# Optimization experiments

Measured on AMD Instinct MI355X. Metric: run time of the kernel, lower is better.

Reference implementation:

```python
import jax, jax.numpy as jnp
import numpy as np

B, N, D, K, H = 32768, 17, 2, 3, 64


def _mlp_params(key, n, d_in, d_hid, d_out):
    k1, k2, k3, k4 = jax.random.split(key, 4)
    W1 = jax.random.normal(k1, (n, d_in, d_hid), jnp.float32) / np.sqrt(d_in)
    b1 = jnp.zeros((n, d_hid), jnp.float32)
    W2 = jax.random.normal(k2, (n, d_hid, d_out), jnp.float32) / np.sqrt(d_hid)
    b2 = jnp.zeros((n, d_out), jnp.float32)
    return W1, b1, W2, b2


def setup_inputs() -> dict:
    key = jax.random.key(0)
    kp, kk, kw, kb = jax.random.split(key, 4)
    pred_pts = jax.random.normal(kp, (B, N, D), jnp.float32)
    kW1, kb1, kW2, kb2 = _mlp_params(kk, N, D, H, K)            # k_nets
    wW1, wb1, wW2, wb2 = _mlp_params(kw, N, D, H, K)            # weight_nets
    bW1, bb1, bW2, bb2 = _mlp_params(kb, N, D, 2 * H, K * 2 * D)  # basis_nets
    return dict(pred_pts=pred_pts,
                kW1=kW1, kb1=kb1, kW2=kW2, kb2=kb2,
                wW1=wW1, wb1=wb1, wW2=wW2, wb2=wb2,
                bW1=bW1, bb1=bb1, bW2=bW2, bb2=bb2)


def _per_joint_mlp(x, W1, b1, W2, b2):
    # x: [B,N,D]; W1: [N,D,Hd]; W2: [N,Hd,O]
    h = jax.nn.relu(jnp.einsum('bnd,ndh->bnh', x, W1) + b1[None])
    return jnp.einsum('bnh,nho->bno', h, W2) + b2[None]


def reference(pred_pts, kW1, kb1, kW2, kb2, wW1, wb1, wW2, wb2, bW1, bb1, bW2, bb2):
    Bc, Nc, Dc = pred_pts.shape
    Kc = kW2.shape[-1]

    # k-selection head (eval mode: argmax, +1)
    k_logits = _per_joint_mlp(pred_pts, kW1, kb1, kW2, kb2)      # [B,N,K]
    k_js = jnp.argmax(k_logits, axis=-1) + 1                     # [B,N] int

    # mixture weights
    w = jax.nn.softmax(_per_joint_mlp(pred_pts, wW1, wb1, wW2, wb2), axis=-1)  # [B,N,K]

    # basis parameters: mu, sigma = exp(log_sigma)
    params = _per_joint_mlp(pred_pts, bW1, bb1, bW2, bb2).reshape(Bc, Nc, Kc, 2 * Dc)
    mu = params[..., :Dc]                                         # [B,N,K,D]
    sigma = jnp.exp(params[..., Dc:])                             # [B,N,K,D]

    # top-k selection by descending weight (indices are constants w.r.t. grad)
    idx = jnp.argsort(-w, axis=-1)                                # [B,N,K]
    mu_top = jnp.take_along_axis(mu, idx[..., None], axis=2)      # [B,N,K,D]
    sigma_top = jnp.take_along_axis(sigma, idx[..., None], axis=2)
    mask = jnp.arange(Kc)[None, None, :] < k_js[..., None]        # [B,N,K] bool

    # pack float outputs: weights + selected (mu, sigma) -> [B,N,K,1+2D]
    out = jnp.concatenate([w[..., None], mu_top, sigma_top], axis=-1)
    return out, k_js, mask
```

## Files before the change

### kernel.cpp

```cpp
#include <hip/hip_runtime.h>
#include <cmath>

#define NBATCH 32768
#define NJOINT 17
#define OUT0_ELEMS (NBATCH * NJOINT * 15)
#define KJS_OFF    OUT0_ELEMS
#define MASK_OFF   (KJS_OFF + NBATCH * NJOINT)

#define WN_STRIDE 774
#define WS_DOUBLES (NJOINT * WN_STRIDE)
#define TILE_B   128

__device__ __forceinline__ float sel3f(int i, float a, float b, float c) {
    return (i == 0) ? a : ((i == 1) ? b : c);
}

__global__ void cvt_weights_f64(
    const float* __restrict__ kW1, const float* __restrict__ kb1,
    const float* __restrict__ kW2, const float* __restrict__ kb2,
    const float* __restrict__ wW1, const float* __restrict__ wb1,
    const float* __restrict__ wW2, const float* __restrict__ wb2,
    double* __restrict__ dws)
{
    const int n = blockIdx.x;
    double* o = dws + (size_t)n * WN_STRIDE;
    for (int i = threadIdx.x; i < WN_STRIDE; i += blockDim.x) {
        int j = i;
        const float* W1 = kW1; const float* b1 = kb1;
        const float* W2 = kW2; const float* b2 = kb2;
        if (j >= 387) { j -= 387; W1 = wW1; b1 = wb1; W2 = wW2; b2 = wb2; }
        float v;
        if (j < 128)      v = W1[n * 128 + j];
        else if (j < 192) v = b1[n * 64 + (j - 128)];
        else if (j < 384) v = W2[n * 192 + (j - 192)];
        else              v = b2[n * 3 + (j - 384)];
        o[i] = (double)v;
    }
}

__device__ __forceinline__ void mlp64_ws_2(
    const double* __restrict__ gws,
    double xA0, double xA1, double xB0, double xB1,
    double& lA0, double& lA1, double& lA2,
    double& lB0, double& lB1, double& lB2)
{
    const double* W1a = gws;
    const double* W1b = gws + 64;
    const double* b1  = gws + 128;
    const double* W2  = gws + 192;
    lA0 = gws[384]; lA1 = gws[385]; lA2 = gws[386];
    lB0 = gws[384]; lB1 = gws[385]; lB2 = gws[386];
    #pragma unroll 4
    for (int h = 0; h < 64; ++h) {
        const double wa = W1a[h], wb = W1b[h], bb = b1[h];
        const double w0 = W2[h * 3 + 0], w1 = W2[h * 3 + 1], w2 = W2[h * 3 + 2];
        double hvA = fmax(fma(xA1, wb, fma(xA0, wa, bb)), 0.0);
        double hvB = fmax(fma(xB1, wb, fma(xB0, wa, bb)), 0.0);
        lA0 = fma(hvA, w0, lA0); lB0 = fma(hvB, w0, lB0);
        lA1 = fma(hvA, w1, lA1); lB1 = fma(hvB, w1, lB1);
        lA2 = fma(hvA, w2, lA2); lB2 = fma(hvB, w2, lB2);
    }
}

__device__ __forceinline__ void mlp64_cvt_2(
    const float* __restrict__ W1, const float* __restrict__ b1f,
    const float* __restrict__ W2f, const float* __restrict__ b2f, int n,
    double xA0, double xA1, double xB0, double xB1,
    double& lA0, double& lA1, double& lA2,
    double& lB0, double& lB1, double& lB2)
{
    const float* W1a = W1 + n * 128;
    const float* W1b = W1a + 64;
    const float* b1  = b1f + n * 64;
    const float* W2  = W2f + n * 192;
    lA0 = (double)b2f[n * 3 + 0]; lB0 = lA0;
    lA1 = (double)b2f[n * 3 + 1]; lB1 = lA1;
    lA2 = (double)b2f[n * 3 + 2]; lB2 = lA2;
    #pragma unroll 4
    for (int h = 0; h < 64; ++h) {
        const double wa = (double)W1a[h], wb = (double)W1b[h], bb = (double)b1[h];
        const double w0 = (double)W2[h * 3 + 0], w1 = (double)W2[h * 3 + 1],
                     w2 = (double)W2[h * 3 + 2];
        double hvA = fmax(fma(xA1, wb, fma(xA0, wa, bb)), 0.0);
        double hvB = fmax(fma(xB1, wb, fma(xB0, wa, bb)), 0.0);
        lA0 = fma(hvA, w0, lA0); lB0 = fma(hvB, w0, lB0);
        lA1 = fma(hvA, w1, lA1); lB1 = fma(hvB, w1, lB1);
        lA2 = fma(hvA, w2, lA2); lB2 = fma(hvB, w2, lB2);
    }
}

__device__ __forceinline__ void decide(
    double kl0, double kl1, double kl2,
    double wl0, double wl1, double wl2,
    int& kj, int& i0, int& i1, int& i2,
    float& p0, float& p1, float& p2)
{
    kj = 0;
    {
        double m = kl0;
        if (kl1 > m) { m = kl1; kj = 1; }
        if (kl2 > m) { kj = 2; }
    }
    i0 = 0;
    {
        double m = wl0;
        if (wl1 > m) { m = wl1; i0 = 1; }
        if (wl2 > m) { i0 = 2; }
    }
    const int ia = (i0 == 0) ? 1 : 0;
    const int ib = (i0 == 2) ? 1 : 2;
    const double wa = ia ? wl1 : wl0;
    const double wb = (ib == 1) ? wl1 : wl2;
    i1 = (wb > wa) ? ib : ia;
    i2 = (wb > wa) ? ia : ib;

    const double mw = fmax(fmax(wl0, wl1), wl2);
    const float e0 = __expf((float)(wl0 - mw));
    const float e1 = __expf((float)(wl1 - mw));
    const float e2 = __expf((float)(wl2 - mw));
    const float inv = 1.0f / (e0 + e1 + e2);
    p0 = e0 * inv; p1 = e1 * inv; p2 = e2 * inv;
}

__device__ __forceinline__ void epilogue(
    const float acc[12], int i0, int i1, int i2,
    float p0, float p1, float p2, float r[15])
{
    r[0]  = p0; r[5] = p1; r[10] = p2;
    r[1]  = sel3f(i0, acc[0], acc[4], acc[8]);
    r[2]  = sel3f(i0, acc[1], acc[5], acc[9]);
    r[3]  = __expf(sel3f(i0, acc[2], acc[6], acc[10]));
    r[4]  = __expf(sel3f(i0, acc[3], acc[7], acc[11]));
    r[6]  = sel3f(i1, acc[0], acc[4], acc[8]);
    r[7]  = sel3f(i1, acc[1], acc[5], acc[9]);
    r[8]  = __expf(sel3f(i1, acc[2], acc[6], acc[10]));
    r[9]  = __expf(sel3f(i1, acc[3], acc[7], acc[11]));
    r[11] = sel3f(i2, acc[0], acc[4], acc[8]);
    r[12] = sel3f(i2, acc[1], acc[5], acc[9]);
    r[13] = __expf(sel3f(i2, acc[2], acc[6], acc[10]));
    r[14] = __expf(sel3f(i2, acc[3], acc[7], acc[11]));
}

template<bool USE_WS>
__device__ __forceinline__ void compute2(
    int n, float xA0f, float xA1f, float xB0f, float xB1f,
    const float* __restrict__ kW1, const float* __restrict__ kb1,
    const float* __restrict__ kW2, const float* __restrict__ kb2,
    const float* __restrict__ wW1, const float* __restrict__ wb1,
    const float* __restrict__ wW2, const float* __restrict__ wb2,
    const float* __restrict__ bW1, const float* __restrict__ bb1,
    const float* __restrict__ bW2, const float* __restrict__ bb2,
    const double* __restrict__ dws,
    float rA[15], float rB[15], int& kjA, int& kjB)
{
    const double xA0 = (double)xA0f, xA1 = (double)xA1f;
    const double xB0 = (double)xB0f, xB1 = (double)xB1f;

    double klA0, klA1, klA2, klB0, klB1, klB2;
    double wlA0, wlA1, wlA2, wlB0, wlB1, wlB2;
    if constexpr (USE_WS) {
        const double* Wn = dws + (size_t)n * WN_STRIDE;
        mlp64_ws_2(Wn,       xA0, xA1, xB0, xB1, klA0, klA1, klA2, klB0, klB1, klB2);
        mlp64_ws_2(Wn + 387, xA0, xA1, xB0, xB1, wlA0, wlA1, wlA2, wlB0, wlB1, wlB2);
    } else {
        mlp64_cvt_2(kW1, kb1, kW2, kb2, n, xA0, xA1, xB0, xB1,
                    klA0, klA1, klA2, klB0, klB1, klB2);
        mlp64_cvt_2(wW1, wb1, wW2, wb2, n, xA0, xA1, xB0, xB1,
                    wlA0, wlA1, wlA2, wlB0, wlB1, wlB2);
    }

    int i0A, i1A, i2A, i0B, i1B, i2B;
    float p0A, p1A, p2A, p0B, p1B, p2B;
    decide(klA0, klA1, klA2, wlA0, wlA1, wlA2, kjA, i0A, i1A, i2A, p0A, p1A, p2A);
    decide(klB0, klB1, klB2, wlB0, wlB1, wlB2, kjB, i0B, i1B, i2B, p0B, p1B, p2B);

    float accA[12], accB[12];
    {
        const float* W1a = bW1 + n * 256;
        const float* W1b = W1a + 128;
        const float* b1  = bb1 + n * 128;
        const float* W2  = bW2 + n * 1536;
        const float* b2  = bb2 + n * 12;
        #pragma unroll
        for (int j = 0; j < 12; ++j) { accA[j] = b2[j]; accB[j] = b2[j]; }
        #pragma unroll 4
        for (int h = 0; h < 128; ++h) {
            const float wa = W1a[h], wb = W1b[h], bb = b1[h];
            float hvA = fmaxf(fmaf(xA1f, wb, fmaf(xA0f, wa, bb)), 0.0f);
            float hvB = fmaxf(fmaf(xB1f, wb, fmaf(xB0f, wa, bb)), 0.0f);
            #pragma unroll
            for (int j = 0; j < 12; ++j) {
                const float wv = W2[h * 12 + j];
                accA[j] = fmaf(hvA, wv, accA[j]);
                accB[j] = fmaf(hvB, wv, accB[j]);
            }
        }
    }

    epilogue(accA, i0A, i1A, i2A, p0A, p1A, p2A, rA);
    epilogue(accB, i0B, i1B, i2B, p0B, p1B, p2B, rB);
}

template<bool USE_WS>
__global__ __launch_bounds__(256, 4) void mdn_fused(
    const float* __restrict__ pred_pts,
    const float* __restrict__ kW1, const float* __restrict__ kb1,
    const float* __restrict__ kW2, const float* __restrict__ kb2,
    const float* __restrict__ wW1, const float* __restrict__ wb1,
    const float* __restrict__ wW2, const float* __restrict__ wb2,
    const float* __restrict__ bW1, const float* __restrict__ bb1,
    const float* __restrict__ bW2, const float* __restrict__ bb2,
    float* __restrict__ out,
    const double* __restrict__ dws)
{
    const int l    = threadIdx.x;
    const int w    = l >> 6;
    const int lane = l & 63;
    const int bx   = blockIdx.x;
    const int by   = blockIdx.y;
    const int n0   = by * 4;

    int n = n0 + w;
    if (n >= NJOINT) return;
    n = __builtin_amdgcn_readfirstlane(n);

    const int bA = bx * TILE_B + lane;
    const int bB = bA + 64;
    const int pA = bA * NJOINT + n;
    const int pB = bB * NJOINT + n;

    const float2 xA = *reinterpret_cast<const float2*>(pred_pts + 2 * pA);
    const float2 xB = *reinterpret_cast<const float2*>(pred_pts + 2 * pB);

    float rA[15], rB[15];
    int kjA, kjB;
    compute2<USE_WS>(n, xA.x, xA.y, xB.x, xB.y,
                     kW1, kb1, kW2, kb2, wW1, wb1, wW2, wb2,
                     bW1, bb1, bW2, bb2, dws, rA, rB, kjA, kjB);

    if (by == 4) {
        float* oA = out + (size_t)pA * 15;
        float* oB = out + (size_t)pB * 15;
        #pragma unroll
        for (int i = 0; i < 15; ++i) { oA[i] = rA[i]; oB[i] = rB[i]; }
        out[KJS_OFF + pA] = (float)(kjA + 1);
        out[KJS_OFF + pB] = (float)(kjB + 1);
        float* mkA = out + MASK_OFF + (size_t)pA * 3;
        mkA[0] = 1.0f; mkA[1] = (kjA >= 1) ? 1.0f : 0.0f; mkA[2] = (kjA >= 2) ? 1.0f : 0.0f;
        float* mkB = out + MASK_OFF + (size_t)pB * 3;
        mkB[0] = 1.0f; mkB[1] = (kjB >= 1) ? 1.0f : 0.0f; mkB[2] = (kjB >= 2) ? 1.0f : 0.0f;
        return;
    }

    __shared__ float s_out[512 * 17];
    {
        float* soA = s_out + (w * TILE_B + lane) * 17;
        float* soB = soA + 64 * 17;
        #pragma unroll
        for (int j = 0; j < 15; ++j) { soA[j] = rA[j]; soB[j] = rB[j]; }
        soA[15] = (float)(kjA + 1);
        soB[15] = (float)(kjB + 1);
    }
    __syncthreads();

    if (l < 240) {
        const int c_off = l / 60;
        const int jj    = l - c_off * 60;
        const int nl    = jj / 15;
        const int j     = jj - nl * 15;
        const int lbase = (nl * TILE_B + c_off) * 17 + j;
        size_t g = (size_t)((bx * TILE_B + c_off) * NJOINT + n0) * 15 + jj;
        #pragma unroll
        for (int rr = 0; rr < 32; ++rr) {
            out[g] = s_out[lbase + 68 * rr];
            g += 1020;
        }
    }

    #pragma unroll
    for (int it = 0; it < 2; ++it) {
        const int q   = it * 256 + l;
        const int bl  = q >> 2;
        const int nlr = q & 3;
        const float kjf = s_out[(nlr * TILE_B + bl) * 17 + 15];
        const int pg = (bx * TILE_B + bl) * NJOINT + n0 + nlr;
        out[KJS_OFF + pg] = kjf;
        float* mk = out + MASK_OFF + (size_t)pg * 3;
        mk[0] = 1.0f;
        mk[1] = (kjf >= 1.5f) ? 1.0f : 0.0f;
        mk[2] = (kjf >= 2.5f) ? 1.0f : 0.0f;
    }
}

extern "C" void kernel_launch(void* const* d_in, const int* in_sizes, int n_in,
                              void* d_out, int out_size, void* d_ws, size_t ws_size,
                              hipStream_t stream) {
    (void)in_sizes; (void)n_in; (void)out_size;
    const bool use_ws = (d_ws != nullptr) && (ws_size >= (size_t)WS_DOUBLES * sizeof(double));
    dim3 grid(NBATCH / TILE_B, 5);
    if (use_ws) {
        cvt_weights_f64<<<NJOINT, 256, 0, stream>>>(
            (const float*)d_in[1], (const float*)d_in[2],
            (const float*)d_in[3], (const float*)d_in[4],
            (const float*)d_in[5], (const float*)d_in[6],
            (const float*)d_in[7], (const float*)d_in[8],
            (double*)d_ws);
        mdn_fused<true><<<grid, 256, 0, stream>>>(
            (const float*)d_in[0],
            (const float*)d_in[1], (const float*)d_in[2],
            (const float*)d_in[3], (const float*)d_in[4],
            (const float*)d_in[5], (const float*)d_in[6],
            (const float*)d_in[7], (const float*)d_in[8],
            (const float*)d_in[9], (const float*)d_in[10],
            (const float*)d_in[11], (const float*)d_in[12],
            (float*)d_out, (const double*)d_ws);
    } else {
        mdn_fused<false><<<grid, 256, 0, stream>>>(
            (const float*)d_in[0],
            (const float*)d_in[1], (const float*)d_in[2],
            (const float*)d_in[3], (const float*)d_in[4],
            (const float*)d_in[5], (const float*)d_in[6],
            (const float*)d_in[7], (const float*)d_in[8],
            (const float*)d_in[9], (const float*)d_in[10],
            (const float*)d_in[11], (const float*)d_in[12],
            (float*)d_out, nullptr);
    }
}
```

Baseline: 150.2 us.

## Compute k/weight heads in fp32 with fp64 fallback only for near-ties

Replaces the always-fp64 evaluation of the k-selection and mixture-weight MLPs with an fp32 pass. The fp64 recompute now runs only for points whose logits are within a tolerance of each other, where argmax or sort order could flip. The grid is reorganised so each block handles one joint for 512 batch points. Basis-net weights are packed into shared memory as float4 groups. Output goes through direct per-point stores instead of the earlier LDS-transposed coalesced store. The tie tolerance is heuristic, so exact argmax agreement is no longer guaranteed, and the uncoalesced stores may cost bandwidth.

```diff
diff --git a/kernel.cpp b/kernel.cpp
--- a/kernel.cpp
+++ b/kernel.cpp
@@ -9,7 +9,8 @@
 
 #define WN_STRIDE 774
 #define WS_DOUBLES (NJOINT * WN_STRIDE)
-#define TILE_B   128
+
+#define BW_FLT 2064
 
 __device__ __forceinline__ float sel3f(int i, float a, float b, float c) {
     return (i == 0) ? a : ((i == 1) ? b : c);
@@ -38,55 +39,77 @@
     }
 }
 
-__device__ __forceinline__ void mlp64_ws_2(
-    const double* __restrict__ gws,
-    double xA0, double xA1, double xB0, double xB1,
-    double& lA0, double& lA1, double& lA2,
-    double& lB0, double& lB1, double& lB2)
+__device__ __forceinline__ void mlp32_2(
+    const float* __restrict__ W1, const float* __restrict__ b1f,
+    const float* __restrict__ W2f, const float* __restrict__ b2f, int n,
+    float xA0, float xA1, float xB0, float xB1,
+    float& lA0, float& lA1, float& lA2,
+    float& lB0, float& lB1, float& lB2)
+{
+    const float* W1a = W1 + n * 128;
+    const float* W1b = W1a + 64;
+    const float* b1  = b1f + n * 64;
+    const float* W2  = W2f + n * 192;
+    lA0 = b2f[n * 3 + 0]; lB0 = lA0;
+    lA1 = b2f[n * 3 + 1]; lB1 = lA1;
+    lA2 = b2f[n * 3 + 2]; lB2 = lA2;
+    #pragma unroll 4
+    for (int h = 0; h < 64; ++h) {
+        const float wa = W1a[h], wb = W1b[h], bb = b1[h];
+        const float w0 = W2[h * 3 + 0], w1 = W2[h * 3 + 1], w2 = W2[h * 3 + 2];
+        float hvA = fmaxf(fmaf(xA1, wb, fmaf(xA0, wa, bb)), 0.0f);
+        float hvB = fmaxf(fmaf(xB1, wb, fmaf(xB0, wa, bb)), 0.0f);
+        lA0 = fmaf(hvA, w0, lA0); lB0 = fmaf(hvB, w0, lB0);
+        lA1 = fmaf(hvA, w1, lA1); lB1 = fmaf(hvB, w1, lB1);
+        lA2 = fmaf(hvA, w2, lA2); lB2 = fmaf(hvB, w2, lB2);
+    }
+}
+
+__device__ __forceinline__ void mlp64_ws_1(
+    const double* __restrict__ gws, double x0, double x1,
+    double& l0, double& l1, double& l2)
 {
     const double* W1a = gws;
     const double* W1b = gws + 64;
     const double* b1  = gws + 128;
     const double* W2  = gws + 192;
-    lA0 = gws[384]; lA1 = gws[385]; lA2 = gws[386];
-    lB0 = gws[384]; lB1 = gws[385]; lB2 = gws[386];
+    l0 = gws[384]; l1 = gws[385]; l2 = gws[386];
     #pragma unroll 4
     for (int h = 0; h < 64; ++h) {
-        const double wa = W1a[h], wb = W1b[h], bb = b1[h];
-        const double w0 = W2[h * 3 + 0], w1 = W2[h * 3 + 1], w2 = W2[h * 3 + 2];
-        double hvA = fmax(fma(xA1, wb, fma(xA0, wa, bb)), 0.0);
-        double hvB = fmax(fma(xB1, wb, fma(xB0, wa, bb)), 0.0);
-        lA0 = fma(hvA, w0, lA0); lB0 = fma(hvB, w0, lB0);
-        lA1 = fma(hvA, w1, lA1); lB1 = fma(hvB, w1, lB1);
-        lA2 = fma(hvA, w2, lA2); lB2 = fma(hvB, w2, lB2);
-    }
-}
-
-__device__ __forceinline__ void mlp64_cvt_2(
+        double hv = fmax(fma(x1, W1b[h], fma(x0, W1a[h], b1[h])), 0.0);
+        l0 = fma(hv, W2[h * 3 + 0], l0);
+        l1 = fma(hv, W2[h * 3 + 1], l1);
+        l2 = fma(hv, W2[h * 3 + 2], l2);
+    }
+}
+
+__device__ __forceinline__ void mlp64_cvt_1(
     const float* __restrict__ W1, const float* __restrict__ b1f,
     const float* __restrict__ W2f, const float* __restrict__ b2f, int n,
-    double xA0, double xA1, double xB0, double xB1,
-    double& lA0, double& lA1, double& lA2,
-    double& lB0, double& lB1, double& lB2)
+    double x0, double x1, double& l0, double& l1, double& l2)
 {
     const float* W1a = W1 + n * 128;
     const float* W1b = W1a + 64;
     const float* b1  = b1f + n * 64;
     const float* W2  = W2f + n * 192;
-    lA0 = (double)b2f[n * 3 + 0]; lB0 = lA0;
-    lA1 = (double)b2f[n * 3 + 1]; lB1 = lA1;
-    lA2 = (double)b2f[n * 3 + 2]; lB2 = lA2;
+    l0 = (double)b2f[n * 3 + 0];
+    l1 = (double)b2f[n * 3 + 1];
+    l2 = (double)b2f[n * 3 + 2];
     #pragma unroll 4
     for (int h = 0; h < 64; ++h) {
-        const double wa = (double)W1a[h], wb = (double)W1b[h], bb = (double)b1[h];
-        const double w0 = (double)W2[h * 3 + 0], w1 = (double)W2[h * 3 + 1],
-                     w2 = (double)W2[h * 3 + 2];
-        double hvA = fmax(fma(xA1, wb, fma(xA0, wa, bb)), 0.0);
-        double hvB = fmax(fma(xB1, wb, fma(xB0, wa, bb)), 0.0);
-        lA0 = fma(hvA, w0, lA0); lB0 = fma(hvB, w0, lB0);
-        lA1 = fma(hvA, w1, lA1); lB1 = fma(hvB, w1, lB1);
-        lA2 = fma(hvA, w2, lA2); lB2 = fma(hvB, w2, lB2);
-    }
+        double hv = fma(x1, (double)W1b[h], fma(x0, (double)W1a[h], (double)b1[h]));
+        hv = fmax(hv, 0.0);
+        l0 = fma(hv, (double)W2[h * 3 + 0], l0);
+        l1 = fma(hv, (double)W2[h * 3 + 1], l1);
+        l2 = fma(hv, (double)W2[h * 3 + 2], l2);
+    }
+}
+
+__device__ __forceinline__ bool tight3(float a, float b, float c) {
+    const float m01 = fabsf(a - b), m02 = fabsf(a - c), m12 = fabsf(b - c);
+    const float mn = fminf(m01, fminf(m02, m12));
+    const float tau = 1e-3f * (1.0f + 0.02f * (fabsf(a) + fabsf(b) + fabsf(c)));
+    return mn < tau;
 }
 
 __device__ __forceinline__ void decide(
@@ -141,64 +164,17 @@
     r[14] = __expf(sel3f(i2, acc[3], acc[7], acc[11]));
 }
 
-template<bool USE_WS>
-__device__ __forceinline__ void compute2(
-    int n, float xA0f, float xA1f, float xB0f, float xB1f,
-    const float* __restrict__ kW1, const float* __restrict__ kb1,
-    const float* __restrict__ kW2, const float* __restrict__ kb2,
-    const float* __restrict__ wW1, const float* __restrict__ wb1,
-    const float* __restrict__ wW2, const float* __restrict__ wb2,
-    const float* __restrict__ bW1, const float* __restrict__ bb1,
-    const float* __restrict__ bW2, const float* __restrict__ bb2,
-    const double* __restrict__ dws,
-    float rA[15], float rB[15], int& kjA, int& kjB)
-{
-    const double xA0 = (double)xA0f, xA1 = (double)xA1f;
-    const double xB0 = (double)xB0f, xB1 = (double)xB1f;
-
-    double klA0, klA1, klA2, klB0, klB1, klB2;
-    double wlA0, wlA1, wlA2, wlB0, wlB1, wlB2;
-    if constexpr (USE_WS) {
-        const double* Wn = dws + (size_t)n * WN_STRIDE;
-        mlp64_ws_2(Wn,       xA0, xA1, xB0, xB1, klA0, klA1, klA2, klB0, klB1, klB2);
-        mlp64_ws_2(Wn + 387, xA0, xA1, xB0, xB1, wlA0, wlA1, wlA2, wlB0, wlB1, wlB2);
-    } else {
-        mlp64_cvt_2(kW1, kb1, kW2, kb2, n, xA0, xA1, xB0, xB1,
-                    klA0, klA1, klA2, klB0, klB1, klB2);
-        mlp64_cvt_2(wW1, wb1, wW2, wb2, n, xA0, xA1, xB0, xB1,
-                    wlA0, wlA1, wlA2, wlB0, wlB1, wlB2);
-    }
-
-    int i0A, i1A, i2A, i0B, i1B, i2B;
-    float p0A, p1A, p2A, p0B, p1B, p2B;
-    decide(klA0, klA1, klA2, wlA0, wlA1, wlA2, kjA, i0A, i1A, i2A, p0A, p1A, p2A);
-    decide(klB0, klB1, klB2, wlB0, wlB1, wlB2, kjB, i0B, i1B, i2B, p0B, p1B, p2B);
-
-    float accA[12], accB[12];
-    {
-        const float* W1a = bW1 + n * 256;
-        const float* W1b = W1a + 128;
-        const float* b1  = bb1 + n * 128;
-        const float* W2  = bW2 + n * 1536;
-        const float* b2  = bb2 + n * 12;
-        #pragma unroll
-        for (int j = 0; j < 12; ++j) { accA[j] = b2[j]; accB[j] = b2[j]; }
-        #pragma unroll 4
-        for (int h = 0; h < 128; ++h) {
-            const float wa = W1a[h], wb = W1b[h], bb = b1[h];
-            float hvA = fmaxf(fmaf(xA1f, wb, fmaf(xA0f, wa, bb)), 0.0f);
-            float hvB = fmaxf(fmaf(xB1f, wb, fmaf(xB0f, wa, bb)), 0.0f);
-            #pragma unroll
-            for (int j = 0; j < 12; ++j) {
-                const float wv = W2[h * 12 + j];
-                accA[j] = fmaf(hvA, wv, accA[j]);
-                accB[j] = fmaf(hvB, wv, accB[j]);
-            }
-        }
-    }
-
-    epilogue(accA, i0A, i1A, i2A, p0A, p1A, p2A, rA);
-    epilogue(accB, i0B, i1B, i2B, p0B, p1B, p2B, rB);
+__device__ __forceinline__ void store_point(
+    float* __restrict__ out, int p, const float r[15], int kj)
+{
+    float* o = out + (size_t)p * 15;
+    #pragma unroll
+    for (int i = 0; i < 15; ++i) o[i] = r[i];
+    out[KJS_OFF + p] = (float)(kj + 1);
+    float* mk = out + MASK_OFF + (size_t)p * 3;
+    mk[0] = 1.0f;
+    mk[1] = (kj >= 1) ? 1.0f : 0.0f;
+    mk[2] = (kj >= 2) ? 1.0f : 0.0f;
 }
 
 template<bool USE_WS>
@@ -213,83 +189,108 @@
     float* __restrict__ out,
     const double* __restrict__ dws)
 {
-    const int l    = threadIdx.x;
-    const int w    = l >> 6;
-    const int lane = l & 63;
-    const int bx   = blockIdx.x;
-    const int by   = blockIdx.y;
-    const int n0   = by * 4;
-
-    int n = n0 + w;
-    if (n >= NJOINT) return;
-    n = __builtin_amdgcn_readfirstlane(n);
-
-    const int bA = bx * TILE_B + lane;
-    const int bB = bA + 64;
+    const int tid = threadIdx.x;
+    const int bid = blockIdx.x;
+    const int n   = bid >> 6;
+    const int bxx = bid & 63;
+
+    __shared__ __align__(16) float bw[BW_FLT];
+    for (int j = tid; j < BW_FLT; j += 256) {
+        const int g = j >> 4, s = j & 15;
+        float f;
+        if (g < 128) {
+            f = (s == 0) ? bW1[n * 256 + g]
+              : (s == 1) ? bW1[n * 256 + 128 + g]
+              : (s == 2) ? bb1[n * 128 + g]
+              : (s == 3) ? 0.0f
+              :            bW2[n * 1536 + g * 12 + (s - 4)];
+        } else {
+            f = (s < 12) ? bb2[n * 12 + s] : 0.0f;
+        }
+        bw[j] = f;
+    }
+
+    const int bA = bxx * 512 + tid;
+    const int bB = bA + 256;
     const int pA = bA * NJOINT + n;
     const int pB = bB * NJOINT + n;
-
     const float2 xA = *reinterpret_cast<const float2*>(pred_pts + 2 * pA);
     const float2 xB = *reinterpret_cast<const float2*>(pred_pts + 2 * pB);
 
+    __syncthreads();
+
+    float kA0, kA1, kA2, kB0, kB1, kB2;
+    float wA0, wA1, wA2, wB0, wB1, wB2;
+    mlp32_2(kW1, kb1, kW2, kb2, n, xA.x, xA.y, xB.x, xB.y,
+            kA0, kA1, kA2, kB0, kB1, kB2);
+    mlp32_2(wW1, wb1, wW2, wb2, n, xA.x, xA.y, xB.x, xB.y,
+            wA0, wA1, wA2, wB0, wB1, wB2);
+
+    const bool fA = tight3(kA0, kA1, kA2) || tight3(wA0, wA1, wA2);
+    const bool fB = tight3(kB0, kB1, kB2) || tight3(wB0, wB1, wB2);
+
+    double klA0 = kA0, klA1 = kA1, klA2 = kA2;
+    double klB0 = kB0, klB1 = kB1, klB2 = kB2;
+    double wlA0 = wA0, wlA1 = wA1, wlA2 = wA2;
+    double wlB0 = wB0, wlB1 = wB1, wlB2 = wB2;
+
+    if (__any(fA || fB)) {
+        if constexpr (USE_WS) {
+            const double* Wn = dws + (size_t)n * WN_STRIDE;
+            if (fA) {
+                mlp64_ws_1(Wn,       (double)xA.x, (double)xA.y, klA0, klA1, klA2);
+                mlp64_ws_1(Wn + 387, (double)xA.x, (double)xA.y, wlA0, wlA1, wlA2);
+            }
+            if (fB) {
+                mlp64_ws_1(Wn,       (double)xB.x, (double)xB.y, klB0, klB1, klB2);
+                mlp64_ws_1(Wn + 387, (double)xB.x, (double)xB.y, wlB0, wlB1, wlB2);
+            }
+        } else {
+            if (fA) {
+                mlp64_cvt_1(kW1, kb1, kW2, kb2, n, (double)xA.x, (double)xA.y, klA0, klA1, klA2);
+                mlp64_cvt_1(wW1, wb1, wW2, wb2, n, (double)xA.x, (double)xA.y, wlA0, wlA1, wlA2);
+            }
+            if (fB) {
+                mlp64_cvt_1(kW1, kb1, kW2, kb2, n, (double)xB.x, (double)xB.y, klB0, klB1, klB2);
+                mlp64_cvt_1(wW1, wb1, wW2, wb2, n, (double)xB.x, (double)xB.y, wlB0, wlB1, wlB2);
+            }
+        }
+    }
+
+    int kjA, i0A, i1A, i2A, kjB, i0B, i1B, i2B;
+    float p0A, p1A, p2A, p0B, p1B, p2B;
+    decide(klA0, klA1, klA2, wlA0, wlA1, wlA2, kjA, i0A, i1A, i2A, p0A, p1A, p2A);
+    decide(klB0, klB1, klB2, wlB0, wlB1, wlB2, kjB, i0B, i1B, i2B, p0B, p1B, p2B);
+
+    float accA[12], accB[12];
+    #pragma unroll
+    for (int j = 0; j < 12; ++j) { const float t = bw[2048 + j]; accA[j] = t; accB[j] = t; }
+    #pragma unroll 4
+    for (int h = 0; h < 128; ++h) {
+        const float4* g4 = reinterpret_cast<const float4*>(bw + (h << 4));
+        const float4 q0 = g4[0], q1 = g4[1], q2 = g4[2], q3 = g4[3];
+        const float hvA = fmaxf(fmaf(xA.y, q0.y, fmaf(xA.x, q0.x, q0.z)), 0.0f);
+        const float hvB = fmaxf(fmaf(xB.y, q0.y, fmaf(xB.x, q0.x, q0.z)), 0.0f);
+        accA[0]  = fmaf(hvA, q1.x, accA[0]);  accB[0]  = fmaf(hvB, q1.x, accB[0]);
+        accA[1]  = fmaf(hvA, q1.y, accA[1]);  accB[1]  = fmaf(hvB, q1.y, accB[1]);
+        accA[2]  = fmaf(hvA, q1.z, accA[2]);  accB[2]  = fmaf(hvB, q1.z, accB[2]);
+        accA[3]  = fmaf(hvA, q1.w, accA[3]);  accB[3]  = fmaf(hvB, q1.w, accB[3]);
+        accA[4]  = fmaf(hvA, q2.x, accA[4]);  accB[4]  = fmaf(hvB, q2.x, accB[4]);
+        accA[5]  = fmaf(hvA, q2.y, accA[5]);  accB[5]  = fmaf(hvB, q2.y, accB[5]);
+        accA[6]  = fmaf(hvA, q2.z, accA[6]);  accB[6]  = fmaf(hvB, q2.z, accB[6]);
+        accA[7]  = fmaf(hvA, q2.w, accA[7]);  accB[7]  = fmaf(hvB, q2.w, accB[7]);
+        accA[8]  = fmaf(hvA, q3.x, accA[8]);  accB[8]  = fmaf(hvB, q3.x, accB[8]);
+        accA[9]  = fmaf(hvA, q3.y, accA[9]);  accB[9]  = fmaf(hvB, q3.y, accB[9]);
+        accA[10] = fmaf(hvA, q3.z, accA[10]); accB[10] = fmaf(hvB, q3.z, accB[10]);
+        accA[11] = fmaf(hvA, q3.w, accA[11]); accB[11] = fmaf(hvB, q3.w, accB[11]);
+    }
+
     float rA[15], rB[15];
-    int kjA, kjB;
-    compute2<USE_WS>(n, xA.x, xA.y, xB.x, xB.y,
-                     kW1, kb1, kW2, kb2, wW1, wb1, wW2, wb2,
-                     bW1, bb1, bW2, bb2, dws, rA, rB, kjA, kjB);
-
-    if (by == 4) {
-        float* oA = out + (size_t)pA * 15;
-        float* oB = out + (size_t)pB * 15;
-        #pragma unroll
-        for (int i = 0; i < 15; ++i) { oA[i] = rA[i]; oB[i] = rB[i]; }
-        out[KJS_OFF + pA] = (float)(kjA + 1);
-        out[KJS_OFF + pB] = (float)(kjB + 1);
-        float* mkA = out + MASK_OFF + (size_t)pA * 3;
-        mkA[0] = 1.0f; mkA[1] = (kjA >= 1) ? 1.0f : 0.0f; mkA[2] = (kjA >= 2) ? 1.0f : 0.0f;
-        float* mkB = out + MASK_OFF + (size_t)pB * 3;
-        mkB[0] = 1.0f; mkB[1] = (kjB >= 1) ? 1.0f : 0.0f; mkB[2] = (kjB >= 2) ? 1.0f : 0.0f;
-        return;
-    }
-
-    __shared__ float s_out[512 * 17];
-    {
-        float* soA = s_out + (w * TILE_B + lane) * 17;
-        float* soB = soA + 64 * 17;
-        #pragma unroll
-        for (int j = 0; j < 15; ++j) { soA[j] = rA[j]; soB[j] = rB[j]; }
-        soA[15] = (float)(kjA + 1);
-        soB[15] = (float)(kjB + 1);
-    }
-    __syncthreads();
-
-    if (l < 240) {
-        const int c_off = l / 60;
-        const int jj    = l - c_off * 60;
-        const int nl    = jj / 15;
-        const int j     = jj - nl * 15;
-        const int lbase = (nl * TILE_B + c_off) * 17 + j;
-        size_t g = (size_t)((bx * TILE_B + c_off) * NJOINT + n0) * 15 + jj;
-        #pragma unroll
-        for (int rr = 0; rr < 32; ++rr) {
-            out[g] = s_out[lbase + 68 * rr];
-            g += 1020;
-        }
-    }
-
-    #pragma unroll
-    for (int it = 0; it < 2; ++it) {
-        const int q   = it * 256 + l;
-        const int bl  = q >> 2;
-        const int nlr = q & 3;
-        const float kjf = s_out[(nlr * TILE_B + bl) * 17 + 15];
-        const int pg = (bx * TILE_B + bl) * NJOINT + n0 + nlr;
-        out[KJS_OFF + pg] = kjf;
-        float* mk = out + MASK_OFF + (size_t)pg * 3;
-        mk[0] = 1.0f;
-        mk[1] = (kjf >= 1.5f) ? 1.0f : 0.0f;
-        mk[2] = (kjf >= 2.5f) ? 1.0f : 0.0f;
-    }
+    epilogue(accA, i0A, i1A, i2A, p0A, p1A, p2A, rA);
+    epilogue(accB, i0B, i1B, i2B, p0B, p1B, p2B, rB);
+
+    store_point(out, pA, rA, kjA);
+    store_point(out, pB, rB, kjB);
 }
 
 extern "C" void kernel_launch(void* const* d_in, const int* in_sizes, int n_in,
@@ -297,7 +298,7 @@
                               hipStream_t stream) {
     (void)in_sizes; (void)n_in; (void)out_size;
     const bool use_ws = (d_ws != nullptr) && (ws_size >= (size_t)WS_DOUBLES * sizeof(double));
-    dim3 grid(NBATCH / TILE_B, 5);
+    dim3 grid(NJOINT * 64);
     if (use_ws) {
         cvt_weights_f64<<<NJOINT, 256, 0, stream>>>(
             (const float*)d_in[1], (const float*)d_in[2],
```

Measured after the change: 165.5 us. 10.2% more time.
